# Kernel tuning notes

Measured on AMD Instinct MI355X. Metric: run time of the kernel, lower is better.

The kernel has to match this reference:

```python
import jax, jax.numpy as jnp
import numpy as np

K_SIZE = 7   # min_kernel_size (Parameter init value, clamped)
DIL = 2      # min_dilation (Parameter init value, clamped)


def conv2d(x, w, b):
    # x: (B, Cin, H, W), w: (Cout, Cin, kh, kw), stride 1, pad 1
    y = jax.lax.conv_general_dilated(
        x, w, window_strides=(1, 1), padding=((1, 1), (1, 1)),
        dimension_numbers=("NCHW", "OIHW", "NCHW"))
    return y + b[None, :, None, None]


def sincos_1d(length, dim, dtype):
    # standard sinusoidal encoding: (length, dim)
    half = dim // 2
    inv_freq = 1.0 / (10000.0 ** (jnp.arange(half, dtype=dtype) * 2.0 / dim))
    ang = jnp.arange(length, dtype=dtype)[:, None] * inv_freq[None, :]
    return jnp.concatenate([jnp.sin(ang), jnp.cos(ang)], axis=-1)


def positional_encoding_2d(H, W, C, dtype):
    # first C//2 channels encode height, last C//2 encode width -> (H, W, C)
    pe_h = sincos_1d(H, C // 2, dtype)  # (H, C/2)
    pe_w = sincos_1d(W, C // 2, dtype)  # (W, C/2)
    pe = jnp.concatenate([
        jnp.broadcast_to(pe_h[:, None, :], (H, W, C // 2)),
        jnp.broadcast_to(pe_w[None, :, :], (H, W, C // 2)),
    ], axis=-1)
    return pe


def na_indices(L, K, D):
    # NATTEN-style dilated neighborhood indices with border clamping.
    # Each position i attends within its dilation group g = i % D.
    i = jnp.arange(L)
    g = i % D
    r = i // D                       # rank within group
    Lg = (L - g + D - 1) // D        # group length
    start = jnp.clip(r - K // 2, 0, Lg - K)
    return g[:, None] + (start[:, None] + jnp.arange(K)[None, :]) * D  # (L, K)


def neighborhood_attention_2d(q, k, v, K, D):
    # q, k: (B, H, W, Cqk); v: (B, H, W, Cv); single head, scale = Cqk**-0.5
    B, H, W, Cqk = q.shape
    scale = jnp.asarray(Cqk, q.dtype) ** -0.5
    idx_h = na_indices(H, K, D)  # (H, K)
    idx_w = na_indices(W, K, D)  # (W, K)
    # gather neighborhood keys/values: (B, H, K, W, K, C)
    kn = k[:, idx_h][:, :, :, idx_w]
    vn = v[:, idx_h][:, :, :, idx_w]
    logits = jnp.einsum('bhwc,bhiwjc->bhwij', q * scale, kn)  # (B,H,W,K,K)
    p = jax.nn.softmax(logits.reshape(B, H, W, K * K), axis=-1)
    p = p.reshape(B, H, W, K, K)
    return jnp.einsum('bhwij,bhiwjc->bhwc', p, vn)


def setup_inputs() -> dict:
    key = jax.random.key(0)
    ks = jax.random.split(key, 4)
    B, Cin, H, W = 2, 64, 96, 96
    Ci, Co = 64, 128
    fan = Cin * 9
    s = (1.0 / fan) ** 0.5
    return {
        "x": jax.random.normal(ks[0], (B, Cin, H, W), dtype=jnp.float32),
        "wq": jax.random.normal(ks[1], (Ci, Cin, 3, 3), dtype=jnp.float32) * s,
        "bq": jnp.zeros((Ci,), dtype=jnp.float32),
        "wk": jax.random.normal(ks[2], (Ci, Cin, 3, 3), dtype=jnp.float32) * s,
        "bk": jnp.zeros((Ci,), dtype=jnp.float32),
        "wv": jax.random.normal(ks[3], (Co, Cin, 3, 3), dtype=jnp.float32) * s,
        "bv": jnp.zeros((Co,), dtype=jnp.float32),
    }


def reference(x, wq, bq, wk, bk, wv, bv):
    # Conv QKV (NCHW), then move to channels-last for attention
    q = jnp.transpose(conv2d(x, wq, bq), (0, 2, 3, 1))  # (B,H,W,Ci)
    k = jnp.transpose(conv2d(x, wk, bk), (0, 2, 3, 1))
    v = jnp.transpose(conv2d(x, wv, bv), (0, 2, 3, 1))  # (B,H,W,Co)
    B, H, W, Ci = q.shape
    pe = positional_encoding_2d(H, W, Ci, q.dtype)       # (H,W,Ci)
    pe_b = jnp.broadcast_to(pe[None], (B, H, W, Ci))
    q = jnp.concatenate([q, pe_b], axis=-1)              # (B,H,W,2*Ci)
    k = jnp.concatenate([k, pe_b], axis=-1)
    return neighborhood_attention_2d(q, k, v, K_SIZE, DIL)
```

## Files before the change

### kernel.cpp

```cpp
#include <hip/hip_runtime.h>
#include <math.h>

#define HWDIM 96
#define NPIX (HWDIM*HWDIM)
#define BATCH 2
#define CIN 64
#define CCAT 128
#define PADW 98

typedef __attribute__((ext_vector_type(8))) short bf16x8;
typedef __attribute__((ext_vector_type(4))) float f32x4;

__device__ __forceinline__ unsigned short f2bf(float f) {
    unsigned u = __builtin_bit_cast(unsigned, f);
    unsigned r = (u + 0x7FFFu + ((u >> 16) & 1u)) >> 16;
    return (unsigned short)r;
}

__global__ __launch_bounds__(256) void prep_kernel(
        const float* __restrict__ x,
        const float* __restrict__ wq, const float* __restrict__ wk,
        const float* __restrict__ wv,
        unsigned short* __restrict__ xp, unsigned short* __restrict__ wbT) {
    int bid = blockIdx.x;
    int tid = threadIdx.x;
    if (bid < 200) {
        int k    = bid & 7;
        int slot = bid >> 3;
        int m    = k & 3;
        int cnt  = 25 - (m >> 1);
        if (slot >= cnt) return;
        int start = 25 * m - (m == 3 ? 1 : 0);
        int b  = k >> 2;
        int hp = start + slot;
        __shared__ float xls[64][97];
        bool interior = (hp >= 1 && hp <= HWDIM);
        if (interior) {
            int h = hp - 1;
            for (int idx = tid; idx < 64 * HWDIM; idx += 256) {
                int ci = idx / HWDIM;
                int w  = idx % HWDIM;
                xls[ci][w] = x[((b * CIN + ci) * HWDIM + h) * HWDIM + w];
            }
        }
        __syncthreads();
        for (int idx = tid; idx < PADW * 64; idx += 256) {
            int wp = idx / 64;
            int ci = idx % 64;
            float v = 0.f;
            if (interior && wp >= 1 && wp <= HWDIM) v = xls[ci][wp - 1];
            xp[((b * PADW + hp) * PADW + wp) * 64 + ci] = f2bf(v);
        }
    } else {
        int base = (bid - 200) * 4096;
        #pragma unroll
        for (int e = 0; e < 16; ++e) {
            int idx = base + e * 256 + tid;
            int t   = idx / (256 * 64);
            int rem = idx % (256 * 64);
            int co  = rem / 64;
            int ci  = rem % 64;
            float val;
            if (co < 64)        val = wq[(co * 64 + ci) * 9 + t];
            else if (co < 128)  val = wk[((co - 64) * 64 + ci) * 9 + t];
            else                val = wv[((co - 128) * 64 + ci) * 9 + t];
            wbT[(t * 256 + co) * 64 + ci] = f2bf(val);
        }
    }
}

__global__ __launch_bounds__(256, 2) void conv_mfma(
        const unsigned short* __restrict__ xp,
        const unsigned short* __restrict__ wbT,
        const float* __restrict__ bq, const float* __restrict__ bk,
        const float* __restrict__ bv,
        unsigned short* __restrict__ Qb, unsigned short* __restrict__ Kb,
        unsigned short* __restrict__ Vb) {
    __shared__ unsigned short xs[3 * 98 * 72];
    int bx      = blockIdx.x;
    int spatial = (bx & 7) * 24 + (bx >> 3);
    int b    = spatial / 96;
    int h    = spatial % 96;
    int co0  = blockIdx.y * 128;
    int tid  = threadIdx.x;

    {
        uint4 rv[10];
        int   ldst[10];
        #pragma unroll
        for (int i = 0; i < 10; ++i) {
            int idx = tid + i * 256;
            bool valid = (i < 9) || (tid < 48);
            int r    = idx / 784;
            int rem  = idx % 784;
            int wp   = rem >> 3;
            int c8   = rem & 7;
            if (valid)
                rv[i] = *(const uint4*)&xp[(((b * PADW) + h + r) * PADW + wp) * 64 + c8 * 8];
            ldst[i] = (r * 98 + wp) * 72 + c8 * 8;
        }
        #pragma unroll
        for (int i = 0; i < 10; ++i) {
            bool valid = (i < 9) || (tid < 48);
            if (valid) *(uint4*)&xs[ldst[i]] = rv[i];
        }
    }
    __syncthreads();

    int lane = tid & 63;
    int wv   = tid >> 6;
    int lw   = lane & 15;
    int ksub = (lane >> 4) * 8;
    int co_t = co0 + wv * 32;

    f32x4 acc[6][2];
    #pragma unroll
    for (int m = 0; m < 6; ++m)
        #pragma unroll
        for (int n = 0; n < 2; ++n) acc[m][n] = (f32x4){0.f, 0.f, 0.f, 0.f};

    #pragma unroll
    for (int half = 0; half < 2; ++half) {
        bf16x8 Bf[9][2];
        #pragma unroll
        for (int t = 0; t < 9; ++t) {
            const unsigned short* bp = wbT + ((t * 256 + co_t + lw) * 64) + half * 32 + ksub;
            Bf[t][0] = *(const bf16x8*)(bp);
            Bf[t][1] = *(const bf16x8*)(bp + 16 * 64);
        }
        #pragma unroll
        for (int t = 0; t < 9; ++t) {
            int kh = t / 3, kw = t % 3;
            const unsigned short* ap = xs + (kh * 98 + lw + kw) * 72 + half * 32 + ksub;
            #pragma unroll
            for (int m = 0; m < 6; ++m) {
                bf16x8 A = *(const bf16x8*)(ap + (m * 16) * 72);
                acc[m][0] = __builtin_amdgcn_mfma_f32_16x16x32_bf16(A, Bf[t][0], acc[m][0], 0, 0, 0);
                acc[m][1] = __builtin_amdgcn_mfma_f32_16x16x32_bf16(A, Bf[t][1], acc[m][1], 0, 0, 0);
            }
        }
    }

    __syncthreads();
    unsigned short* xs2 = xs;
    #pragma unroll
    for (int n = 0; n < 2; ++n) {
        int co_f = co_t + n * 16 + lw;
        float bval;
        if (co_f < 64)       bval = bq[co_f];
        else if (co_f < 128) bval = bk[co_f - 64];
        else                 bval = bv[co_f - 128];
        int chl = wv * 32 + n * 16 + lw;
        #pragma unroll
        for (int m = 0; m < 6; ++m) {
            int px = m * 16 + ((lane >> 4) << 2);
            #pragma unroll
            for (int r = 0; r < 4; ++r)
                xs2[(px + r) * 136 + chl] = f2bf(acc[m][n][r] + bval);
        }
    }
    __syncthreads();

    #pragma unroll
    for (int e = 0; e < 6; ++e) {
        int i   = tid + e * 256;
        int px  = i >> 4;
        int seg = i & 15;
        uint4 v = *(uint4*)&xs2[px * 136 + seg * 8];
        int pix = b * NPIX + h * HWDIM + px;
        int chl = seg * 8;
        if (co0 == 0) {
            if (chl < 64) *(uint4*)&Qb[pix * CCAT + chl]        = v;
            else          *(uint4*)&Kb[pix * CCAT + (chl - 64)] = v;
        } else {
            *(uint4*)&Vb[pix * CCAT + chl] = v;
        }
    }

    if (blockIdx.y == 0) {
        #pragma unroll
        for (int e = 0; e < 24; ++e) {
            int i  = tid + e * 256;
            int c  = i & 63;
            int w  = i >> 6;
            int pos = (c < 32) ? h : w;
            int j   = c & 15;
            float f   = exp2f(-(float)j * 0.83048202372184059f);
            float ang = (float)pos * f;
            float val = ((c & 16) == 0) ? __sinf(ang) : __cosf(ang);
            unsigned short bvv = f2bf(val);
            int pix = b * NPIX + h * HWDIM + w;
            Qb[pix * CCAT + 64 + c] = bvv;
            Kb[pix * CCAT + 64 + c] = bvv;
        }
    }
}

#define KPAD 136
#define LGP  114

__global__ __launch_bounds__(256, 3) void natt_mfma(
        const unsigned short* __restrict__ Qb,
        const unsigned short* __restrict__ Kb,
        const unsigned short* __restrict__ Vb,
        float* __restrict__ out) {
    __shared__ unsigned short Vt[128 * KPAD];
    __shared__ unsigned short Pb[16 * KPAD];
    __shared__ float Lg[16 * LGP];

    int bid  = blockIdx.x;
    int xcd  = bid & 7;
    int slot = bid >> 3;
    int s3   = slot % 3;
    int rest = slot / 3;
    int code = xcd * 3 + s3;
    int b  = code / 12;
    int th = code % 12;
    int tw = rest % 12;
    int gg = rest / 12;
    int gh = gg & 1;
    int gw = gg >> 1;

    int rh0 = th * 4, rw0 = tw * 4;
    int base_h = min(max(rh0 - 3, 0), 41);
    int base_w = min(max(rw0 - 3, 0), 41);
    int tid = threadIdx.x;
    int lane = tid & 63;
    int wv   = tid >> 6;
    int lw   = lane & 15;
    int ks8  = (lane >> 4) * 8;

    uint4 va[4], vb2[4];
    int   vdst[4];
    #pragma unroll
    for (int j = 0; j < 4; ++j) {
        int c = tid + j * 256;
        bool valid = (j < 3) || (tid < 32);
        int pp = c >> 4, c8 = c & 15;
        int px0 = pp * 2, px1 = px0 + 1;
        int ih0 = px0 / 10, iw0 = px0 - ih0 * 10;
        int ih1 = px1 / 10, iw1 = px1 - ih1 * 10;
        int gp0 = b * NPIX + (gh + 2 * min(base_h + ih0, 47)) * HWDIM + (gw + 2 * min(base_w + iw0, 47));
        int gp1 = b * NPIX + (gh + 2 * min(base_h + ih1, 47)) * HWDIM + (gw + 2 * min(base_w + iw1, 47));
        if (valid) {
            va[j]  = *(const uint4*)(Vb + gp0 * CCAT + c8 * 8);
            vb2[j] = *(const uint4*)(Vb + gp1 * CCAT + c8 * 8);
        }
        vdst[j] = (c8 * 8) * KPAD + (px0 ^ ((c8 & 7) << 3));
    }

    for (int i = tid; i < 1024; i += 256) {
        int row = i >> 3, sg = i & 7;
        *(uint4*)(Vt + row * KPAD + 64 + sg * 8) = (uint4){0, 0, 0, 0};
    }

    const float scale = 0.08838834764831845f;
    {
        int qi = lw >> 2, qj = lw & 3;
        const unsigned short* qsrc = Qb +
            ((b * NPIX + (gh + 2 * (rh0 + qi)) * HWDIM + (gw + 2 * (rw0 + qj))) * CCAT) + ks8;
        bf16x8 A0 = *(const bf16x8*)(qsrc);
        bf16x8 A1 = *(const bf16x8*)(qsrc + 32);
        bf16x8 A2 = *(const bf16x8*)(qsrc + 64);
        bf16x8 A3 = *(const bf16x8*)(qsrc + 96);

        #pragma unroll
        for (int tt = 0; tt < 2; ++tt) {
            int tile = wv + tt * 4;
            if (tile < 7) {
                int px = min(tile * 16 + lw, 99);
                int ih = px / 10, iw = px - ih * 10;
                const unsigned short* ksrc = Kb +
                    ((b * NPIX + (gh + 2 * min(base_h + ih, 47)) * HWDIM
                               + (gw + 2 * min(base_w + iw, 47))) * CCAT) + ks8;
                bf16x8 B0 = *(const bf16x8*)(ksrc);
                bf16x8 B1 = *(const bf16x8*)(ksrc + 32);
                bf16x8 B2 = *(const bf16x8*)(ksrc + 64);
                bf16x8 B3 = *(const bf16x8*)(ksrc + 96);
                f32x4 acc = (f32x4){0.f, 0.f, 0.f, 0.f};
                __builtin_amdgcn_s_setprio(1);
                acc = __builtin_amdgcn_mfma_f32_16x16x32_bf16(A0, B0, acc, 0, 0, 0);
                acc = __builtin_amdgcn_mfma_f32_16x16x32_bf16(A1, B1, acc, 0, 0, 0);
                acc = __builtin_amdgcn_mfma_f32_16x16x32_bf16(A2, B2, acc, 0, 0, 0);
                acc = __builtin_amdgcn_mfma_f32_16x16x32_bf16(A3, B3, acc, 0, 0, 0);
                __builtin_amdgcn_s_setprio(0);
                #pragma unroll
                for (int r = 0; r < 4; ++r) {
                    int m = (lane >> 4) * 4 + r;
                    Lg[m * LGP + tile * 16 + lw] = acc[r] * scale;
                }
            }
        }
    }
    __syncthreads();

    #pragma unroll
    for (int j = 0; j < 4; ++j) {
        bool valid = (j < 3) || (tid < 32);
        if (valid) {
            unsigned short* vp = Vt + vdst[j];
            uint4 v0 = va[j], v1 = vb2[j];
            *(unsigned*)(vp + 0 * KPAD) = (v0.x & 0xFFFFu) | (v1.x << 16);
            *(unsigned*)(vp + 1 * KPAD) = (v0.x >> 16)     | (v1.x & 0xFFFF0000u);
            *(unsigned*)(vp + 2 * KPAD) = (v0.y & 0xFFFFu) | (v1.y << 16);
            *(unsigned*)(vp + 3 * KPAD) = (v0.y >> 16)     | (v1.y & 0xFFFF0000u);
            *(unsigned*)(vp + 4 * KPAD) = (v0.z & 0xFFFFu) | (v1.z << 16);
            *(unsigned*)(vp + 5 * KPAD) = (v0.z >> 16)     | (v1.z & 0xFFFF0000u);
            *(unsigned*)(vp + 6 * KPAD) = (v0.w & 0xFFFFu) | (v1.w << 16);
            *(unsigned*)(vp + 7 * KPAD) = (v0.w >> 16)     | (v1.w & 0xFFFF0000u);
        }
    }

    int q   = tid >> 4, k16 = tid & 15;
    {
        int qi  = q >> 2, qj = q & 3;
        int rh  = rh0 + qi, rw = rw0 + qj;
        int oh  = min(max(rh - 3, 0), 41) - base_h;
        int ow  = min(max(rw - 3, 0), 41) - base_w;

        float ev[4];
        int   en[4];
        float mx = -1e30f;
        #pragma unroll
        for (int u = 0; u < 4; ++u) {
            int idx = k16 + u * 16;
            if (idx < 49) {
                int i = idx / 7, j = idx - i * 7;
                int n = (oh + i) * 10 + ow + j;
                en[u] = n;
                float l = Lg[q * LGP + n];
                ev[u] = l;
                mx = fmaxf(mx, l);
            } else { en[u] = -1; ev[u] = 0.f; }
        }
        #pragma unroll
        for (int off = 8; off > 0; off >>= 1) mx = fmaxf(mx, __shfl_xor(mx, off));
        float s = 0.f;
        #pragma unroll
        for (int u = 0; u < 4; ++u)
            if (en[u] >= 0) { ev[u] = __expf(ev[u] - mx); s += ev[u]; }
        #pragma unroll
        for (int off = 8; off > 0; off >>= 1) s += __shfl_xor(s, off);
        float rs = 1.0f / s;
        *(uint4*)(Pb + q * KPAD + k16 * 8) = (uint4){0, 0, 0, 0};
        #pragma unroll
        for (int u = 0; u < 4; ++u)
            if (en[u] >= 0) Pb[q * KPAD + en[u]] = f2bf(ev[u] * rs);
    }
    __syncthreads();

    bf16x8 A4[4];
    #pragma unroll
    for (int kk = 0; kk < 4; ++kk)
        A4[kk] = *(const bf16x8*)(Pb + lw * KPAD + kk * 32 + ks8);

    __builtin_amdgcn_s_setprio(1);
    #pragma unroll
    for (int tt = 0; tt < 2; ++tt) {
        int tile = wv * 2 + tt;
        int row  = tile * 16 + lw;
        int sw   = ((row >> 3) & 7) << 3;
        const unsigned short* vrow = Vt + row * KPAD;
        f32x4 acc = (f32x4){0.f, 0.f, 0.f, 0.f};
        #pragma unroll
        for (int kk = 0; kk < 4; ++kk) {
            bf16x8 Bf = *(const bf16x8*)(vrow + ((kk * 32 + ks8) ^ sw));
            acc = __builtin_amdgcn_mfma_f32_16x16x32_bf16(A4[kk], Bf, acc, 0, 0, 0);
        }
        int ch = row;
        #pragma unroll
        for (int r = 0; r < 4; ++r) {
            int qq = (lane >> 4) * 4 + r;
            int qi = qq >> 2, qj = qq & 3;
            int gp = b * NPIX + (gh + 2 * (rh0 + qi)) * HWDIM + (gw + 2 * (rw0 + qj));
            out[gp * CCAT + ch] = acc[r];
        }
    }
    __builtin_amdgcn_s_setprio(0);
}

extern "C" void kernel_launch(void* const* d_in, const int* in_sizes, int n_in,
                              void* d_out, int out_size, void* d_ws, size_t ws_size,
                              hipStream_t stream) {
    const float* x  = (const float*)d_in[0];
    const float* wq = (const float*)d_in[1];
    const float* bq = (const float*)d_in[2];
    const float* wk = (const float*)d_in[3];
    const float* bk = (const float*)d_in[4];
    const float* wv = (const float*)d_in[5];
    const float* bv = (const float*)d_in[6];

    unsigned short* ws = (unsigned short*)d_ws;
    unsigned short* Qb  = ws;
    unsigned short* Kb  = Qb + BATCH * NPIX * CCAT;
    unsigned short* Vb  = Kb + BATCH * NPIX * CCAT;
    unsigned short* xp  = Vb + BATCH * NPIX * CCAT;
    unsigned short* wbT = xp + BATCH * PADW * PADW * 64;

    hipLaunchKernelGGL(prep_kernel, dim3(236), dim3(256), 0, stream,
                       x, wq, wk, wv, xp, wbT);
    hipLaunchKernelGGL(conv_mfma, dim3(192, 2), dim3(256), 0, stream,
                       xp, wbT, bq, bk, bv, Qb, Kb, Vb);
    hipLaunchKernelGGL(natt_mfma, dim3(1152), dim3(256), 0, stream,
                       Qb, Kb, Vb, (float*)d_out);
}
```

Before: 42.52 us.

## Fuse input/weight prep into conv kernel with flag-based weight sync

```diff
diff --git a/kernel.cpp b/kernel.cpp
--- a/kernel.cpp
+++ b/kernel.cpp
@@ -6,7 +6,6 @@
 #define BATCH 2
 #define CIN 64
 #define CCAT 128
-#define PADW 98
 
 typedef __attribute__((ext_vector_type(8))) short bf16x8;
 typedef __attribute__((ext_vector_type(4))) float f32x4;
@@ -17,63 +16,13 @@
     return (unsigned short)r;
 }
 
-__global__ __launch_bounds__(256) void prep_kernel(
+__global__ __launch_bounds__(256, 2) void conv_all(
         const float* __restrict__ x,
         const float* __restrict__ wq, const float* __restrict__ wk,
         const float* __restrict__ wv,
-        unsigned short* __restrict__ xp, unsigned short* __restrict__ wbT) {
-    int bid = blockIdx.x;
-    int tid = threadIdx.x;
-    if (bid < 200) {
-        int k    = bid & 7;
-        int slot = bid >> 3;
-        int m    = k & 3;
-        int cnt  = 25 - (m >> 1);
-        if (slot >= cnt) return;
-        int start = 25 * m - (m == 3 ? 1 : 0);
-        int b  = k >> 2;
-        int hp = start + slot;
-        __shared__ float xls[64][97];
-        bool interior = (hp >= 1 && hp <= HWDIM);
-        if (interior) {
-            int h = hp - 1;
-            for (int idx = tid; idx < 64 * HWDIM; idx += 256) {
-                int ci = idx / HWDIM;
-                int w  = idx % HWDIM;
-                xls[ci][w] = x[((b * CIN + ci) * HWDIM + h) * HWDIM + w];
-            }
-        }
-        __syncthreads();
-        for (int idx = tid; idx < PADW * 64; idx += 256) {
-            int wp = idx / 64;
-            int ci = idx % 64;
-            float v = 0.f;
-            if (interior && wp >= 1 && wp <= HWDIM) v = xls[ci][wp - 1];
-            xp[((b * PADW + hp) * PADW + wp) * 64 + ci] = f2bf(v);
-        }
-    } else {
-        int base = (bid - 200) * 4096;
-        #pragma unroll
-        for (int e = 0; e < 16; ++e) {
-            int idx = base + e * 256 + tid;
-            int t   = idx / (256 * 64);
-            int rem = idx % (256 * 64);
-            int co  = rem / 64;
-            int ci  = rem % 64;
-            float val;
-            if (co < 64)        val = wq[(co * 64 + ci) * 9 + t];
-            else if (co < 128)  val = wk[((co - 64) * 64 + ci) * 9 + t];
-            else                val = wv[((co - 128) * 64 + ci) * 9 + t];
-            wbT[(t * 256 + co) * 64 + ci] = f2bf(val);
-        }
-    }
-}
-
-__global__ __launch_bounds__(256, 2) void conv_mfma(
-        const unsigned short* __restrict__ xp,
-        const unsigned short* __restrict__ wbT,
         const float* __restrict__ bq, const float* __restrict__ bk,
         const float* __restrict__ bv,
+        unsigned short* __restrict__ wbT, unsigned* __restrict__ flag,
         unsigned short* __restrict__ Qb, unsigned short* __restrict__ Kb,
         unsigned short* __restrict__ Vb) {
     __shared__ unsigned short xs[3 * 98 * 72];
@@ -84,34 +33,69 @@
     int co0  = blockIdx.y * 128;
     int tid  = threadIdx.x;
 
-    {
-        uint4 rv[10];
-        int   ldst[10];
-        #pragma unroll
-        for (int i = 0; i < 10; ++i) {
-            int idx = tid + i * 256;
-            bool valid = (i < 9) || (tid < 48);
-            int r    = idx / 784;
-            int rem  = idx % 784;
-            int wp   = rem >> 3;
-            int c8   = rem & 7;
-            if (valid)
-                rv[i] = *(const uint4*)&xp[(((b * PADW) + h + r) * PADW + wp) * 64 + c8 * 8];
-            ldst[i] = (r * 98 + wp) * 72 + c8 * 8;
-        }
-        #pragma unroll
-        for (int i = 0; i < 10; ++i) {
-            bool valid = (i < 9) || (tid < 48);
-            if (valid) *(uint4*)&xs[ldst[i]] = rv[i];
-        }
+    if (blockIdx.y == 0 && bx < 36) {
+        int base = bx * 2048;
+        #pragma unroll
+        for (int e = 0; e < 8; ++e) {
+            int idx2 = base + e * 256 + tid;
+            int t    = idx2 / 8192;
+            int rem  = idx2 % 8192;
+            int co   = rem >> 5;
+            int ci2  = rem & 31;
+            int ci   = ci2 * 2;
+            float v0, v1;
+            if (co < 64)       { v0 = wq[(co * 64 + ci) * 9 + t];        v1 = wq[(co * 64 + ci + 1) * 9 + t]; }
+            else if (co < 128) { v0 = wk[((co - 64) * 64 + ci) * 9 + t]; v1 = wk[((co - 64) * 64 + ci + 1) * 9 + t]; }
+            else               { v0 = wv[((co - 128) * 64 + ci) * 9 + t]; v1 = wv[((co - 128) * 64 + ci + 1) * 9 + t]; }
+            unsigned pack = (unsigned)f2bf(v0) | ((unsigned)f2bf(v1) << 16);
+            __hip_atomic_store((unsigned*)&wbT[(t * 256 + co) * 64 + ci], pack,
+                               __ATOMIC_RELAXED, __HIP_MEMORY_SCOPE_AGENT);
+        }
+        __syncthreads();
+        if (tid == 0)
+            __hip_atomic_fetch_add(flag, 1u, __ATOMIC_RELEASE, __HIP_MEMORY_SCOPE_AGENT);
+    }
+
+    #pragma unroll
+    for (int g = 0; g < 18; ++g) {
+        int i   = tid + g * 256;
+        int r   = i / 1536;
+        int rem = i % 1536;
+        int ci  = rem / 24;
+        int p4  = rem % 24;
+        int iy  = h - 1 + r;
+        float4 v = make_float4(0.f, 0.f, 0.f, 0.f);
+        if (iy >= 0 && iy < HWDIM)
+            v = *(const float4*)&x[((b * CIN + ci) * HWDIM + iy) * HWDIM + p4 * 4];
+        int bse = (r * 98 + 1 + p4 * 4) * 72 + ci;
+        xs[bse]       = f2bf(v.x);
+        xs[bse + 72]  = f2bf(v.y);
+        xs[bse + 144] = f2bf(v.z);
+        xs[bse + 216] = f2bf(v.w);
+    }
+    if (tid < 192) {
+        #pragma unroll
+        for (int e = 0; e < 2; ++e) {
+            int ii  = tid + e * 192;
+            int r   = ii / 128;
+            int rem = ii % 128;
+            int ci  = rem >> 1;
+            int px  = (rem & 1) ? 97 : 0;
+            xs[(r * 98 + px) * 72 + ci] = 0;
+        }
+    }
+
+    if (tid == 0) {
+        while (__hip_atomic_load(flag, __ATOMIC_ACQUIRE, __HIP_MEMORY_SCOPE_AGENT) < 36u)
+            __builtin_amdgcn_s_sleep(8);
     }
     __syncthreads();
 
     int lane = tid & 63;
-    int wv   = tid >> 6;
+    int wv_  = tid >> 6;
     int lw   = lane & 15;
     int ksub = (lane >> 4) * 8;
-    int co_t = co0 + wv * 32;
+    int co_t = co0 + wv_ * 32;
 
     f32x4 acc[6][2];
     #pragma unroll
@@ -150,7 +134,7 @@
         if (co_f < 64)       bval = bq[co_f];
         else if (co_f < 128) bval = bk[co_f - 64];
         else                 bval = bv[co_f - 128];
-        int chl = wv * 32 + n * 16 + lw;
+        int chl = wv_ * 32 + n * 16 + lw;
         #pragma unroll
         for (int m = 0; m < 6; ++m) {
             int px = m * 16 + ((lane >> 4) << 2);
@@ -394,13 +378,12 @@
     unsigned short* Qb  = ws;
     unsigned short* Kb  = Qb + BATCH * NPIX * CCAT;
     unsigned short* Vb  = Kb + BATCH * NPIX * CCAT;
-    unsigned short* xp  = Vb + BATCH * NPIX * CCAT;
-    unsigned short* wbT = xp + BATCH * PADW * PADW * 64;
-
-    hipLaunchKernelGGL(prep_kernel, dim3(236), dim3(256), 0, stream,
-                       x, wq, wk, wv, xp, wbT);
-    hipLaunchKernelGGL(conv_mfma, dim3(192, 2), dim3(256), 0, stream,
-                       xp, wbT, bq, bk, bv, Qb, Kb, Vb);
+    unsigned short* wbT = Vb + BATCH * NPIX * CCAT;
+    unsigned*       flag = (unsigned*)(wbT + 147456);
+
+    hipMemsetAsync(flag, 0, 4, stream);
+    hipLaunchKernelGGL(conv_all, dim3(192, 2), dim3(256), 0, stream,
+                       x, wq, wk, wv, bq, bk, bv, wbT, flag, Qb, Kb, Vb);
     hipLaunchKernelGGL(natt_mfma, dim3(1152), dim3(256), 0, stream,
                        Qb, Kb, Vb, (float*)d_out);
 }
```

Measured after the change: 48.52 us. +14.1%, slower.
